# Kernel optimization log

Measured on AMD Instinct MI355X. Metric: run time of the kernel, lower is better.

The kernel has to match this reference:

```python
import jax, jax.numpy as jnp
import numpy as np

B, T, OBS, H, LAT = 512, 512, 64, 256, 16
NEG_SLOPE = 0.01  # flax nn.leaky_relu default


def _glorot(key, shape):
    fan_in, fan_out = shape[0], shape[-1]
    s = jnp.sqrt(6.0 / (fan_in + fan_out))
    return jax.random.uniform(key, shape, jnp.float32, -s, s)


def setup_inputs() -> dict:
    key = jax.random.key(0)
    ks = jax.random.split(key, 12)
    x = jax.random.normal(ks[0], (B, T, OBS), jnp.float32)
    lengths = jax.random.randint(ks[1], (B,), T // 4, T + 1)
    mask = jnp.arange(T)[None, :] < lengths[:, None]  # [B,T] bool, prefix-valid
    return {
        "x": x,
        "mask": mask,
        # encoder params
        "Wip": _glorot(ks[2], (OBS, H)), "bip": jnp.zeros((H,)),
        "Wi_e": _glorot(ks[3], (H, 4 * H)), "Wh_e": _glorot(ks[4], (H, 4 * H)),
        "b_e": jnp.zeros((4 * H,)),
        "Wlp": _glorot(ks[5], (H, LAT)), "blp": jnp.zeros((LAT,)),
        # decoder params
        "Wle": _glorot(ks[6], (LAT, H)), "ble": jnp.zeros((H,)),
        "Wi_d": _glorot(ks[7], (H, 4 * H)), "Wh_d": _glorot(ks[8], (H, 4 * H)),
        "b_d": jnp.zeros((4 * H,)),
        "Wop": _glorot(ks[9], (H, OBS)), "bop": jnp.zeros((OBS,)),
    }


def _lstm_step(c, h, x_t, Wi, Wh, b):
    # flax OptimizedLSTMCell: fused gates, order i, f, g, o
    z = x_t @ Wi + h @ Wh + b  # [B, 4H]
    i, f, g, o = jnp.split(z, 4, axis=-1)
    new_c = jax.nn.sigmoid(f) * c + jax.nn.sigmoid(i) * jnp.tanh(g)
    new_h = jax.nn.sigmoid(o) * jnp.tanh(new_c)
    return new_c, new_h


def _forward(x, mask, Wip, bip, Wi_e, Wh_e, b_e, Wlp, blp,
             Wle, ble, Wi_d, Wh_d, b_d, Wop, bop):
    # ---- Encoder ----
    xp = jax.nn.leaky_relu(x @ Wip + bip, NEG_SLOPE)  # [B,T,H]
    xs = (jnp.swapaxes(xp, 0, 1), jnp.swapaxes(mask, 0, 1)[:, :, None])  # [T,B,H],[T,B,1]

    def enc_step(carry, inp):
        c, h = carry
        x_t, m_t = inp
        nc, nh = _lstm_step(c, h, x_t, Wi_e, Wh_e, b_e)
        # masked carry update (MaskedLSTMCell)
        return (jnp.where(m_t, nc, c), jnp.where(m_t, nh, h)), None

    init = (jnp.zeros((x.shape[0], Wh_e.shape[0]), x.dtype),
            jnp.zeros((x.shape[0], Wh_e.shape[0]), x.dtype))
    (c_f, h_f), _ = jax.lax.scan(enc_step, init, xs)
    latent = h_f @ Wlp + blp  # [B,LAT]

    ctx = jax.nn.leaky_relu(latent @ Wle + ble, NEG_SLOPE)  # [B,H]

    def dec_step(carry, _):
        c, h = carry
        nc, nh = _lstm_step(c, h, h, Wi_d, Wh_d, b_d)
        pred = nh @ Wop + bop
        return (nc, nh), pred

    _, recon = jax.lax.scan(dec_step, (ctx, ctx), None, length=T)  # [T,B,OBS]
    recon = jnp.swapaxes(recon, 0, 1)  # [B,T,OBS]
    return recon, latent


def reference(x, mask, Wip, bip, Wi_e, Wh_e, b_e, Wlp, blp,
              Wle, ble, Wi_d, Wh_d, b_d, Wop, bop):
    return _forward(x, mask, Wip, bip, Wi_e, Wh_e, b_e, Wlp, blp,
                    Wle, ble, Wi_d, Wh_d, b_d, Wop, bop)
```

## Files before the change

kernel.cpp:

```cpp
#include <hip/hip_runtime.h>

typedef unsigned short u16;
typedef unsigned long long u64;
typedef float f32x4 __attribute__((ext_vector_type(4)));
typedef __bf16 bf16x8 __attribute__((ext_vector_type(8)));

#define NT_ 512
#define LD 264
#define SPIN_GUARD 100000

__device__ __forceinline__ u16 f2bf(float f) {
  unsigned u = __builtin_bit_cast(unsigned, f);
  u += 0x7FFFu + ((u >> 16) & 1u);
  return (u16)(u >> 16);
}
__device__ __forceinline__ float bf2f(u16 h) {
  unsigned u = ((unsigned)h) << 16;
  return __builtin_bit_cast(float, u);
}
__device__ __forceinline__ f32x4 splat4(float b) { f32x4 v = {b, b, b, b}; return v; }
__device__ __forceinline__ bf16x8 asb(uint4 v) { return __builtin_bit_cast(bf16x8, v); }
__device__ __forceinline__ float sigf(float v) { return 1.0f / (1.0f + exp2f(-1.44269504f * v)); }
__device__ __forceinline__ float tanhf_(float v) { float e = exp2f(2.88539008f * v); return 1.0f - 2.0f / (e + 1.0f); }

__device__ __forceinline__ u64 gld64(const u64* p) {
  return __hip_atomic_load(p, __ATOMIC_RELAXED, __HIP_MEMORY_SCOPE_AGENT);
}
__device__ __forceinline__ void gst64(u64* p, u64 v) {
  __hip_atomic_store(p, v, __ATOMIC_RELAXED, __HIP_MEMORY_SCOPE_AGENT);
}
__device__ __forceinline__ int gld32(const int* p) {
  return __hip_atomic_load(p, __ATOMIC_RELAXED, __HIP_MEMORY_SCOPE_AGENT);
}
__device__ __forceinline__ void gst32(int* p, int v) {
  __hip_atomic_store(p, v, __ATOMIC_RELAXED, __HIP_MEMORY_SCOPE_AGENT);
}

__global__ void k_pack_g(const float* __restrict__ src, const float* __restrict__ src2,
                         u16* __restrict__ dst) {
  int e = blockIdx.x * 256 + threadIdx.x;
  int j = e & 7, lane = (e >> 3) & 63, g = (e >> 9) & 3, ks = (e >> 11) & 7;
  int w = (e >> 14) & 3, s = (e >> 16) & 3;
  int k = ks * 32 + ((lane >> 4) << 3) + j;
  int col = g * 256 + s * 64 + w * 16 + (lane & 15);
  float v = src[k * 1024 + col];
  if (src2) v += src2[k * 1024 + col];
  dst[e] = f2bf(v);
}
__global__ void k_pack_wip(const float* __restrict__ Wip, u16* __restrict__ dst) {
  int e = blockIdx.x * 256 + threadIdx.x;
  int j = e & 7, lane = (e >> 3) & 63, n = (e >> 9) & 3, ks2 = (e >> 11) & 1, w = (e >> 12) & 3;
  int k = ks2 * 32 + ((lane >> 4) << 3) + j;
  int col = w * 64 + n * 16 + (lane & 15);
  dst[e] = f2bf(Wip[k * 256 + col]);
}
__global__ void k_pack_wop(const float* __restrict__ Wop, u16* __restrict__ dst) {
  int e = blockIdx.x * 256 + threadIdx.x;
  int j = e & 7, lane = (e >> 3) & 63, ks = (e >> 9) & 7, s = (e >> 12) & 3;
  int k = ks * 32 + ((lane >> 4) << 3) + j;
  int col = s * 16 + (lane & 15);
  dst[e] = f2bf(Wop[k * 64 + col]);
}

__global__ void k_lens(const unsigned char* __restrict__ mask, int* __restrict__ skeys) {
  int b = threadIdx.x;
  bool u8 = (mask[1] | mask[2] | mask[3]) != 0;
  int s = 0;
  if (u8) { const unsigned char* row = mask + b * NT_; for (int t = 0; t < NT_; t++) s += row[t] ? 1 : 0; }
  else { const int* row = (const int*)mask + b * NT_; for (int t = 0; t < NT_; t++) s += row[t] ? 1 : 0; }
  skeys[b] = s * 1024 + b;
}

__global__ void k_sort(int* __restrict__ skeys) {
  __shared__ int sk[512];
  int tid = threadIdx.x;
  sk[tid] = skeys[tid];
  __syncthreads();
  for (int k = 2; k <= 512; k <<= 1)
    for (int j = k >> 1; j > 0; j >>= 1) {
      int ixj = tid ^ j;
      if (ixj > tid) {
        int a = sk[tid], b = sk[ixj];
        bool up = ((tid & k) == 0);
        if ((a > b) == up) { sk[tid] = b; sk[ixj] = a; }
      }
      __syncthreads();
    }
  skeys[tid] = sk[tid];
}

__global__ void k_zero(int* __restrict__ flags) { flags[threadIdx.x] = 0; }

__global__ __launch_bounds__(256, 1) void k_rec3(
    const float* __restrict__ x,
    const u16* __restrict__ whe_p, const u16* __restrict__ wie_p,
    const u16* __restrict__ wd_p, const u16* __restrict__ wip_p,
    const u16* __restrict__ wop_p,
    const float* __restrict__ bip, const float* __restrict__ be,
    const float* __restrict__ Wlp, const float* __restrict__ blp,
    const float* __restrict__ Wle, const float* __restrict__ ble,
    const float* __restrict__ bd, const float* __restrict__ bop,
    const int* __restrict__ skeys,
    u64* __restrict__ hpub, int* __restrict__ eflag, int* __restrict__ dflag,
    float* __restrict__ out) {
  __shared__ __align__(16) u16 hx[16 * LD];
  __shared__ __align__(16) u16 xps[16 * LD];
  __shared__ __align__(16) u16 xbuf[16 * 72];
  __shared__ int ob_s[16], len_s[16];
  __shared__ float lat_s[256];

  const int tid = threadIdx.x;
  const int w = tid >> 6, lane = tid & 63, q = lane >> 4, n16 = lane & 15;
  const int b = blockIdx.x;
  const int g = (b & 7) + ((b >> 5) << 3);
  const int s = (b >> 3) & 3;

  if (tid < 16) {
    int v = skeys[g * 16 + tid];
    ob_s[tid] = v & 1023;
    len_s[tid] = v >> 10;
  }
  for (int i = tid; i < 16 * LD; i += 256) hx[i] = 0;
  __syncthreads();
  int maxlen = 0;
#pragma unroll
  for (int i = 0; i < 16; i++) maxlen = len_s[i] > maxlen ? len_s[i] : maxlen;
  int mylen[4];
#pragma unroll
  for (int r = 0; r < 4; r++) mylen[r] = len_s[q * 4 + r];

  const uint4* whe4 = (const uint4*)whe_p;
  const uint4* wie4 = (const uint4*)wie_p;
  const uint4* wip4 = (const uint4*)wip_p;
  uint4 wfh[32], wfx[32], wipf[8];
#pragma unroll
  for (int f = 0; f < 32; f++) wfh[f] = whe4[((s * 4 + w) * 32 + f) * 64 + lane];
#pragma unroll
  for (int f = 0; f < 32; f++) wfx[f] = wie4[((s * 4 + w) * 32 + f) * 64 + lane];
#pragma unroll
  for (int f = 0; f < 8; f++) wipf[f] = wip4[(w * 8 + f) * 64 + lane];

  float be_r[4], bipr[4];
#pragma unroll
  for (int gt = 0; gt < 4; gt++) be_r[gt] = be[gt * 256 + s * 64 + w * 16 + n16];
#pragma unroll
  for (int n = 0; n < 4; n++) bipr[n] = bip[w * 64 + n * 16 + n16];

  float creg[4], hreg[4];
#pragma unroll
  for (int r = 0; r < 4; r++) { creg[r] = 0.f; hreg[r] = 0.f; }

  const char* hxb = (const char*)hx;
  const char* xpsb = (const char*)xps;
  u64* hpg = hpub + (u64)g * 2048;
  int* efl = eflag + g * 4;
  int* dfl = dflag + g * 4;
  const int xr = tid >> 4, xc = tid & 15;
  const int pubw = (w * 16 + n16) * 4 + q;
  const int mycol = s * 64 + w * 16 + n16;

  for (int t = 0; t < maxlen; t++) {
    float4 xv = ((const float4*)x)[((size_t)ob_s[xr] * NT_ + t) * 16 + xc];
    {
      u64 pv = (u64)f2bf(xv.x) | ((u64)f2bf(xv.y) << 16) |
               ((u64)f2bf(xv.z) << 32) | ((u64)f2bf(xv.w) << 48);
      *(u64*)&xbuf[xr * 72 + xc * 4] = pv;
    }
    __syncthreads();
    f32x4 xacc[4];
#pragma unroll
    for (int n = 0; n < 4; n++) xacc[n] = splat4(bipr[n]);
#pragma unroll
    for (int ks2 = 0; ks2 < 2; ks2++) {
      bf16x8 a = *(const bf16x8*)((const char*)xbuf + n16 * 144 + ks2 * 64 + q * 16);
#pragma unroll
      for (int n = 0; n < 4; n++)
        xacc[n] = __builtin_amdgcn_mfma_f32_16x16x32_bf16(a, asb(wipf[ks2 * 4 + n]), xacc[n], 0, 0, 0);
    }
#pragma unroll
    for (int n = 0; n < 4; n++)
#pragma unroll
      for (int r = 0; r < 4; r++) {
        float v = xacc[n][r];
        v = v >= 0.f ? v : 0.01f * v;
        xps[(q * 4 + r) * LD + w * 64 + n * 16 + n16] = f2bf(v);
      }
    __syncthreads();
    f32x4 acc[4];
#pragma unroll
    for (int gt = 0; gt < 4; gt++) acc[gt] = splat4(be_r[gt]);
#pragma unroll
    for (int ks = 0; ks < 8; ks++) {
      bf16x8 a = *(const bf16x8*)(xpsb + n16 * (LD * 2) + ks * 64 + q * 16);
#pragma unroll
      for (int gt = 0; gt < 4; gt++)
        acc[gt] = __builtin_amdgcn_mfma_f32_16x16x32_bf16(a, asb(wfx[ks * 4 + gt]), acc[gt], 0, 0, 0);
    }
    if (t > 0) {
      if (tid < 4 && tid != s) {
        int gdn = 0;
        while (gld32(&efl[tid]) < t && ++gdn < SPIN_GUARD) {}
      }
      __syncthreads();
      const u64* src = hpg + (u64)(t & 1) * 1024;
#pragma unroll
      for (int e3 = 0; e3 < 3; e3++) {
        int sidx = e3 + (e3 >= s);
        u64 v = gld64(&src[sidx * 256 + tid]);
        int cc = sidx * 64 + (tid >> 2), qq = tid & 3;
#pragma unroll
        for (int r = 0; r < 4; r++) hx[(qq * 4 + r) * LD + cc] = (u16)(v >> (16 * r));
      }
    }
    __syncthreads();
#pragma unroll
    for (int ks = 0; ks < 8; ks++) {
      bf16x8 a = *(const bf16x8*)(hxb + n16 * (LD * 2) + ks * 64 + q * 16);
#pragma unroll
      for (int gt = 0; gt < 4; gt++)
        acc[gt] = __builtin_amdgcn_mfma_f32_16x16x32_bf16(a, asb(wfh[ks * 4 + gt]), acc[gt], 0, 0, 0);
    }
    u16 hb[4];
#pragma unroll
    for (int r = 0; r < 4; r++) {
      float i_ = sigf(acc[0][r]);
      float f_ = sigf(acc[1][r]);
      float g_ = tanhf_(acc[2][r]);
      float o_ = sigf(acc[3][r]);
      float nc = f_ * creg[r] + i_ * g_;
      float nh = o_ * tanhf_(nc);
      bool upd = t < mylen[r];
      creg[r] = upd ? nc : creg[r];
      hreg[r] = upd ? nh : hreg[r];
      hb[r] = f2bf(hreg[r]);
    }
    {
      u64 pv = (u64)hb[0] | ((u64)hb[1] << 16) | ((u64)hb[2] << 32) | ((u64)hb[3] << 48);
      gst64(&hpg[(u64)((t + 1) & 1) * 1024 + s * 256 + pubw], pv);
    }
    __syncthreads();
#pragma unroll
    for (int r = 0; r < 4; r++) hx[(q * 4 + r) * LD + mycol] = hb[r];
    __syncthreads();
    if (tid == 0) gst32(&efl[s], t + 1);
  }

  if (tid < 4 && tid != s) {
    int gdn = 0;
    while (gld32(&efl[tid]) < maxlen && ++gdn < SPIN_GUARD) {}
  }
  __syncthreads();
  {
    const u64* src = hpg + (u64)(maxlen & 1) * 1024;
#pragma unroll
    for (int e3 = 0; e3 < 3; e3++) {
      int sidx = e3 + (e3 >= s);
      u64 v = gld64(&src[sidx * 256 + tid]);
      int cc = sidx * 64 + (tid >> 2), qq = tid & 3;
#pragma unroll
      for (int r = 0; r < 4; r++) hx[(qq * 4 + r) * LD + cc] = (u16)(v >> (16 * r));
    }
  }
  __syncthreads();
  if (tid == 0) gst32(&dfl[s], 1);

  {
    int m = tid >> 4, j = tid & 15;
    float acc_ = blp[j];
    for (int k = 0; k < 256; k++) acc_ = fmaf(bf2f(hx[m * LD + k]), Wlp[k * 16 + j], acc_);
    if (s == 0) out[16777216 + ob_s[m] * 16 + j] = acc_;
    lat_s[m * 16 + j] = acc_;
  }
  __syncthreads();
  for (int i = tid; i < 4096; i += 256) {
    int m = i >> 8, c = i & 255;
    float v = ble[c];
#pragma unroll
    for (int k = 0; k < 16; k++) v = fmaf(lat_s[m * 16 + k], Wle[k * 256 + c], v);
    v = v >= 0.f ? v : 0.01f * v;
    hx[m * LD + c] = f2bf(v);
  }
  __syncthreads();
#pragma unroll
  for (int r = 0; r < 4; r++) {
    hreg[r] = bf2f(hx[(q * 4 + r) * LD + mycol]);
    creg[r] = hreg[r];
  }

  const uint4* wd4 = (const uint4*)wd_p;
  const uint4* wop4 = (const uint4*)wop_p;
#pragma unroll
  for (int f = 0; f < 32; f++) wfh[f] = wd4[((s * 4 + w) * 32 + f) * 64 + lane];
#pragma unroll
  for (int f = 0; f < 8; f++) wfx[f] = wop4[(s * 8 + f) * 64 + lane];
  float bd_r[4];
#pragma unroll
  for (int gt = 0; gt < 4; gt++) bd_r[gt] = bd[gt * 256 + s * 64 + w * 16 + n16];
  float bop_r = bop[s * 16 + n16];
  int orow[4];
#pragma unroll
  for (int r = 0; r < 4; r++) orow[r] = ob_s[q * 4 + r] << 15;

  if (tid < 4 && tid != s) {
    int gdn = 0;
    while (gld32(&dfl[tid]) < 1 && ++gdn < SPIN_GUARD) {}
  }
  __syncthreads();

  for (int d = 0; d < NT_; d++) {
    if (d > 0) {
      if (tid < 4 && tid != s) {
        int gdn = 0;
        while (gld32(&dfl[tid]) < d + 1 && ++gdn < SPIN_GUARD) {}
      }
      __syncthreads();
      const u64* src = hpg + (u64)(d & 1) * 1024;
#pragma unroll
      for (int e3 = 0; e3 < 3; e3++) {
        int sidx = e3 + (e3 >= s);
        u64 v = gld64(&src[sidx * 256 + tid]);
        int cc = sidx * 64 + (tid >> 2), qq = tid & 3;
#pragma unroll
        for (int r = 0; r < 4; r++) hx[(qq * 4 + r) * LD + cc] = (u16)(v >> (16 * r));
      }
    }
    __syncthreads();
    f32x4 pacc = splat4(0.f);
#pragma unroll
    for (int ks = 0; ks < 8; ks++) {
      bf16x8 a = *(const bf16x8*)(hxb + n16 * (LD * 2) + ks * 64 + q * 16);
      pacc = __builtin_amdgcn_mfma_f32_16x16x32_bf16(a, asb(wfx[ks]), pacc, 0, 0, 0);
    }
    if (w == 0 && d > 0) {
#pragma unroll
      for (int r = 0; r < 4; r++)
        out[orow[r] + ((d - 1) << 6) + (s << 4) + n16] = pacc[r] + bop_r;
    }
    f32x4 acc[4];
#pragma unroll
    for (int gt = 0; gt < 4; gt++) acc[gt] = splat4(bd_r[gt]);
#pragma unroll
    for (int ks = 0; ks < 8; ks++) {
      bf16x8 a = *(const bf16x8*)(hxb + n16 * (LD * 2) + ks * 64 + q * 16);
#pragma unroll
      for (int gt = 0; gt < 4; gt++)
        acc[gt] = __builtin_amdgcn_mfma_f32_16x16x32_bf16(a, asb(wfh[ks * 4 + gt]), acc[gt], 0, 0, 0);
    }
    u16 hb[4];
#pragma unroll
    for (int r = 0; r < 4; r++) {
      float i_ = sigf(acc[0][r]);
      float f_ = sigf(acc[1][r]);
      float g_ = tanhf_(acc[2][r]);
      float o_ = sigf(acc[3][r]);
      float nc = f_ * creg[r] + i_ * g_;
      creg[r] = nc;
      hreg[r] = o_ * tanhf_(nc);
      hb[r] = f2bf(hreg[r]);
    }
    {
      u64 pv = (u64)hb[0] | ((u64)hb[1] << 16) | ((u64)hb[2] << 32) | ((u64)hb[3] << 48);
      gst64(&hpg[(u64)((d + 1) & 1) * 1024 + s * 256 + pubw], pv);
    }
    __syncthreads();
#pragma unroll
    for (int r = 0; r < 4; r++) hx[(q * 4 + r) * LD + mycol] = hb[r];
    __syncthreads();
    if (tid == 0) gst32(&dfl[s], d + 2);
  }
  if (tid < 4 && tid != s) {
    int gdn = 0;
    while (gld32(&dfl[tid]) < NT_ + 1 && ++gdn < SPIN_GUARD) {}
  }
  __syncthreads();
  {
    const u64* src = hpg;
#pragma unroll
    for (int e3 = 0; e3 < 3; e3++) {
      int sidx = e3 + (e3 >= s);
      u64 v = gld64(&src[sidx * 256 + tid]);
      int cc = sidx * 64 + (tid >> 2), qq = tid & 3;
#pragma unroll
      for (int r = 0; r < 4; r++) hx[(qq * 4 + r) * LD + cc] = (u16)(v >> (16 * r));
    }
  }
  __syncthreads();
  if (w == 0) {
    f32x4 pacc = splat4(0.f);
#pragma unroll
    for (int ks = 0; ks < 8; ks++) {
      bf16x8 a = *(const bf16x8*)(hxb + n16 * (LD * 2) + ks * 64 + q * 16);
      pacc = __builtin_amdgcn_mfma_f32_16x16x32_bf16(a, asb(wfx[ks]), pacc, 0, 0, 0);
    }
#pragma unroll
    for (int r = 0; r < 4; r++)
      out[orow[r] + (511 << 6) + (s << 4) + n16] = pacc[r] + bop_r;
  }
}

#define OFF_WHE 0ull
#define OFF_WIE 524288ull
#define OFF_WD 1048576ull
#define OFF_WIP 1572864ull
#define OFF_WOP 1605632ull
#define OFF_HPUB 1638400ull
#define OFF_EFLAG 2162688ull
#define OFF_DFLAG 2163200ull
#define OFF_SKEYS 2163712ull
#define MIN_WS 2165760ull

extern "C" void kernel_launch(void* const* d_in, const int* in_sizes, int n_in,
                              void* d_out, int out_size, void* d_ws, size_t ws_size,
                              hipStream_t stream) {
  const float* x = (const float*)d_in[0];
  const unsigned char* mask = (const unsigned char*)d_in[1];
  const float* Wip = (const float*)d_in[2];
  const float* bip = (const float*)d_in[3];
  const float* Wie = (const float*)d_in[4];
  const float* Whe = (const float*)d_in[5];
  const float* be = (const float*)d_in[6];
  const float* Wlp = (const float*)d_in[7];
  const float* blp = (const float*)d_in[8];
  const float* Wle = (const float*)d_in[9];
  const float* ble = (const float*)d_in[10];
  const float* Wid = (const float*)d_in[11];
  const float* Whd = (const float*)d_in[12];
  const float* bd = (const float*)d_in[13];
  const float* Wop = (const float*)d_in[14];
  const float* bop = (const float*)d_in[15];
  float* out = (float*)d_out;
  char* ws = (char*)d_ws;

  if (ws_size < MIN_WS) return;

  u16* whe_p = (u16*)(ws + OFF_WHE);
  u16* wie_p = (u16*)(ws + OFF_WIE);
  u16* wd_p = (u16*)(ws + OFF_WD);
  u16* wip_p = (u16*)(ws + OFF_WIP);
  u16* wop_p = (u16*)(ws + OFF_WOP);
  u64* hpub = (u64*)(ws + OFF_HPUB);
  int* eflag = (int*)(ws + OFF_EFLAG);
  int* dflag = (int*)(ws + OFF_DFLAG);
  int* skeys = (int*)(ws + OFF_SKEYS);

  k_pack_g<<<1024, 256, 0, stream>>>(Whe, nullptr, whe_p);
  k_pack_g<<<1024, 256, 0, stream>>>(Wie, nullptr, wie_p);
  k_pack_g<<<1024, 256, 0, stream>>>(Wid, Whd, wd_p);
  k_pack_wip<<<64, 256, 0, stream>>>(Wip, wip_p);
  k_pack_wop<<<64, 256, 0, stream>>>(Wop, wop_p);
  k_lens<<<1, 512, 0, stream>>>(mask, skeys);
  k_sort<<<1, 512, 0, stream>>>(skeys);
  k_zero<<<1, 256, 0, stream>>>(eflag);

  k_rec3<<<128, 256, 0, stream>>>(x, whe_p, wie_p, wd_p, wip_p, wop_p,
                                  bip, be, Wlp, blp, Wle, ble, bd, bop,
                                  skeys, hpub, eflag, dflag, out);
}
```

Before: 3.405 ms.

## Replace flag-based inter-block sync with tagged hidden-state polling

Removes the separate per-step encoder and decoder flag arrays and instead embeds a step tag in the upper 16 bits of each published bf16 hidden value, so consumers poll the data itself with cache-bypassing dwordx4 loads. This drops one flag store, one flag poll and several block-wide barriers per timestep in the latency-bound recurrence. Barriers become raw s_barrier with only an lgkmcnt wait, and the next x row is prefetched one step ahead. The cost is twice the publish traffic, since each value is now 32-bit. Correctness relies on the tag and the sc0/sc1 coherence bits, and on the zeroed buffer never matching a live tag.

```diff
diff --git a/kernel.cpp b/kernel.cpp
--- a/kernel.cpp
+++ b/kernel.cpp
@@ -1,9 +1,11 @@
 #include <hip/hip_runtime.h>
 
 typedef unsigned short u16;
+typedef unsigned u32;
 typedef unsigned long long u64;
 typedef float f32x4 __attribute__((ext_vector_type(4)));
 typedef __bf16 bf16x8 __attribute__((ext_vector_type(8)));
+typedef u32 u32x4 __attribute__((ext_vector_type(4)));
 
 #define NT_ 512
 #define LD 264
@@ -23,17 +25,35 @@
 __device__ __forceinline__ float sigf(float v) { return 1.0f / (1.0f + exp2f(-1.44269504f * v)); }
 __device__ __forceinline__ float tanhf_(float v) { float e = exp2f(2.88539008f * v); return 1.0f - 2.0f / (e + 1.0f); }
 
-__device__ __forceinline__ u64 gld64(const u64* p) {
-  return __hip_atomic_load(p, __ATOMIC_RELAXED, __HIP_MEMORY_SCOPE_AGENT);
-}
-__device__ __forceinline__ void gst64(u64* p, u64 v) {
-  __hip_atomic_store(p, v, __ATOMIC_RELAXED, __HIP_MEMORY_SCOPE_AGENT);
-}
-__device__ __forceinline__ int gld32(const int* p) {
-  return __hip_atomic_load(p, __ATOMIC_RELAXED, __HIP_MEMORY_SCOPE_AGENT);
-}
-__device__ __forceinline__ void gst32(int* p, int v) {
-  __hip_atomic_store(p, v, __ATOMIC_RELAXED, __HIP_MEMORY_SCOPE_AGENT);
+__device__ __forceinline__ void barL() {
+  asm volatile("s_waitcnt lgkmcnt(0)\n\ts_barrier" ::: "memory");
+}
+
+__device__ __forceinline__ void pub4(u32* p, u32x4 v) {
+  asm volatile("global_store_dwordx4 %0, %1, off sc0 sc1" :: "v"(p), "v"(v) : "memory");
+}
+
+__device__ __forceinline__ void poll3(const u32* a0, const u32* a1, const u32* a2,
+                                      u32 tg, u32x4& r0, u32x4& r1, u32x4& r2) {
+  int gdn = 0;
+  while (true) {
+    u32x4 t0, t1, t2;
+    asm volatile(
+        "global_load_dwordx4 %0, %3, off sc0 sc1\n\t"
+        "global_load_dwordx4 %1, %4, off sc0 sc1\n\t"
+        "global_load_dwordx4 %2, %5, off sc0 sc1\n\t"
+        "s_waitcnt vmcnt(0)"
+        : "=&v"(t0), "=&v"(t1), "=&v"(t2)
+        : "v"(a0), "v"(a1), "v"(a2)
+        : "memory");
+    bool ok = (t0[0] >> 16) == tg && (t0[1] >> 16) == tg &&
+              (t0[2] >> 16) == tg && (t0[3] >> 16) == tg &&
+              (t1[0] >> 16) == tg && (t1[1] >> 16) == tg &&
+              (t1[2] >> 16) == tg && (t1[3] >> 16) == tg &&
+              (t2[0] >> 16) == tg && (t2[1] >> 16) == tg &&
+              (t2[2] >> 16) == tg && (t2[3] >> 16) == tg;
+    if (ok || ++gdn >= SPIN_GUARD) { r0 = t0; r1 = t1; r2 = t2; return; }
+  }
 }
 
 __global__ void k_pack_g(const float* __restrict__ src, const float* __restrict__ src2,
@@ -89,9 +109,13 @@
   skeys[tid] = sk[tid];
 }
 
-__global__ void k_zero(int* __restrict__ flags) { flags[threadIdx.x] = 0; }
-
-__global__ __launch_bounds__(256, 1) void k_rec3(
+__global__ void k_zero_hpub(u32* __restrict__ hp) {
+  int i = blockIdx.x * 256 + threadIdx.x;
+  u32x4 z = {0u, 0u, 0u, 0u};
+  pub4(hp + (size_t)i * 4, z);
+}
+
+__global__ __launch_bounds__(256, 1) void k_rec4(
     const float* __restrict__ x,
     const u16* __restrict__ whe_p, const u16* __restrict__ wie_p,
     const u16* __restrict__ wd_p, const u16* __restrict__ wip_p,
@@ -101,8 +125,7 @@
     const float* __restrict__ Wle, const float* __restrict__ ble,
     const float* __restrict__ bd, const float* __restrict__ bop,
     const int* __restrict__ skeys,
-    u64* __restrict__ hpub, int* __restrict__ eflag, int* __restrict__ dflag,
-    float* __restrict__ out) {
+    u32* __restrict__ hpub, float* __restrict__ out) {
   __shared__ __align__(16) u16 hx[16 * LD];
   __shared__ __align__(16) u16 xps[16 * LD];
   __shared__ __align__(16) u16 xbuf[16 * 72];
@@ -152,21 +175,44 @@
 
   const char* hxb = (const char*)hx;
   const char* xpsb = (const char*)xps;
-  u64* hpg = hpub + (u64)g * 2048;
-  int* efl = eflag + g * 4;
-  int* dfl = dflag + g * 4;
-  const int xr = tid >> 4, xc = tid & 15;
-  const int pubw = (w * 16 + n16) * 4 + q;
+  u32* hp32 = hpub + (size_t)g * 8192;
+  const int p0 = (s == 0) ? 1 : 0;
+  const int p1 = (s <= 1) ? 2 : 1;
+  const int p2 = (s <= 2) ? 3 : 2;
+  const int widx = ((tid >> 2) << 4) + ((tid & 3) << 2);
+  const int ccl = tid >> 2, qq = tid & 3;
+  const int cc0 = p0 * 64 + ccl, cc1 = p1 * 64 + ccl, cc2 = p2 * 64 + ccl;
+  u32* pubp = hp32 + s * 1024 + ((w * 16 + n16) << 4) + (q << 2);
   const int mycol = s * 64 + w * 16 + n16;
 
+#define SCAT3()                                  \
+  do {                                           \
+    hx[(qq * 4 + 0) * LD + cc0] = (u16)r0[0];    \
+    hx[(qq * 4 + 1) * LD + cc0] = (u16)r0[1];    \
+    hx[(qq * 4 + 2) * LD + cc0] = (u16)r0[2];    \
+    hx[(qq * 4 + 3) * LD + cc0] = (u16)r0[3];    \
+    hx[(qq * 4 + 0) * LD + cc1] = (u16)r1[0];    \
+    hx[(qq * 4 + 1) * LD + cc1] = (u16)r1[1];    \
+    hx[(qq * 4 + 2) * LD + cc1] = (u16)r1[2];    \
+    hx[(qq * 4 + 3) * LD + cc1] = (u16)r1[3];    \
+    hx[(qq * 4 + 0) * LD + cc2] = (u16)r2[0];    \
+    hx[(qq * 4 + 1) * LD + cc2] = (u16)r2[1];    \
+    hx[(qq * 4 + 2) * LD + cc2] = (u16)r2[2];    \
+    hx[(qq * 4 + 3) * LD + cc2] = (u16)r2[3];    \
+  } while (0)
+
+  const float4* xr4 = (const float4*)x + (size_t)ob_s[tid >> 4] * 8192 + (tid & 15);
+  float4 xv = xr4[0];
+
   for (int t = 0; t < maxlen; t++) {
-    float4 xv = ((const float4*)x)[((size_t)ob_s[xr] * NT_ + t) * 16 + xc];
     {
       u64 pv = (u64)f2bf(xv.x) | ((u64)f2bf(xv.y) << 16) |
                ((u64)f2bf(xv.z) << 32) | ((u64)f2bf(xv.w) << 48);
-      *(u64*)&xbuf[xr * 72 + xc * 4] = pv;
-    }
-    __syncthreads();
+      *(u64*)&xbuf[(tid >> 4) * 72 + (tid & 15) * 4] = pv;
+    }
+    int tn = (t + 1 < maxlen) ? t + 1 : t;
+    float4 xnx = xr4[(size_t)tn * 16];
+    barL();
     f32x4 xacc[4];
 #pragma unroll
     for (int n = 0; n < 4; n++) xacc[n] = splat4(bipr[n]);
@@ -185,7 +231,7 @@
         v = v >= 0.f ? v : 0.01f * v;
         xps[(q * 4 + r) * LD + w * 64 + n * 16 + n16] = f2bf(v);
       }
-    __syncthreads();
+    barL();
     f32x4 acc[4];
 #pragma unroll
     for (int gt = 0; gt < 4; gt++) acc[gt] = splat4(be_r[gt]);
@@ -197,22 +243,13 @@
         acc[gt] = __builtin_amdgcn_mfma_f32_16x16x32_bf16(a, asb(wfx[ks * 4 + gt]), acc[gt], 0, 0, 0);
     }
     if (t > 0) {
-      if (tid < 4 && tid != s) {
-        int gdn = 0;
-        while (gld32(&efl[tid]) < t && ++gdn < SPIN_GUARD) {}
-      }
-      __syncthreads();
-      const u64* src = hpg + (u64)(t & 1) * 1024;
-#pragma unroll
-      for (int e3 = 0; e3 < 3; e3++) {
-        int sidx = e3 + (e3 >= s);
-        u64 v = gld64(&src[sidx * 256 + tid]);
-        int cc = sidx * 64 + (tid >> 2), qq = tid & 3;
-#pragma unroll
-        for (int r = 0; r < 4; r++) hx[(qq * 4 + r) * LD + cc] = (u16)(v >> (16 * r));
-      }
-    }
-    __syncthreads();
+      const u32* bp = hp32 + ((t & 1) << 12);
+      u32x4 r0, r1, r2;
+      poll3(bp + p0 * 1024 + widx, bp + p1 * 1024 + widx, bp + p2 * 1024 + widx,
+            (u32)t, r0, r1, r2);
+      SCAT3();
+    }
+    barL();
 #pragma unroll
     for (int ks = 0; ks < 8; ks++) {
       bf16x8 a = *(const bf16x8*)(hxb + n16 * (LD * 2) + ks * 64 + q * 16);
@@ -235,34 +272,24 @@
       hb[r] = f2bf(hreg[r]);
     }
     {
-      u64 pv = (u64)hb[0] | ((u64)hb[1] << 16) | ((u64)hb[2] << 32) | ((u64)hb[3] << 48);
-      gst64(&hpg[(u64)((t + 1) & 1) * 1024 + s * 256 + pubw], pv);
-    }
-    __syncthreads();
+      u32 tgw = (u32)(t + 1) << 16;
+      u32x4 pv = {tgw | hb[0], tgw | hb[1], tgw | hb[2], tgw | hb[3]};
+      pub4(pubp + (((t + 1) & 1) << 12), pv);
+    }
+    barL();
 #pragma unroll
     for (int r = 0; r < 4; r++) hx[(q * 4 + r) * LD + mycol] = hb[r];
-    __syncthreads();
-    if (tid == 0) gst32(&efl[s], t + 1);
-  }
-
-  if (tid < 4 && tid != s) {
-    int gdn = 0;
-    while (gld32(&efl[tid]) < maxlen && ++gdn < SPIN_GUARD) {}
-  }
-  __syncthreads();
+    xv = xnx;
+  }
+
   {
-    const u64* src = hpg + (u64)(maxlen & 1) * 1024;
-#pragma unroll
-    for (int e3 = 0; e3 < 3; e3++) {
-      int sidx = e3 + (e3 >= s);
-      u64 v = gld64(&src[sidx * 256 + tid]);
-      int cc = sidx * 64 + (tid >> 2), qq = tid & 3;
-#pragma unroll
-      for (int r = 0; r < 4; r++) hx[(qq * 4 + r) * LD + cc] = (u16)(v >> (16 * r));
-    }
-  }
-  __syncthreads();
-  if (tid == 0) gst32(&dfl[s], 1);
+    const u32* bp = hp32 + ((maxlen & 1) << 12);
+    u32x4 r0, r1, r2;
+    poll3(bp + p0 * 1024 + widx, bp + p1 * 1024 + widx, bp + p2 * 1024 + widx,
+          (u32)maxlen, r0, r1, r2);
+    SCAT3();
+  }
+  barL();
 
   {
     int m = tid >> 4, j = tid & 15;
@@ -300,31 +327,17 @@
   int orow[4];
 #pragma unroll
   for (int r = 0; r < 4; r++) orow[r] = ob_s[q * 4 + r] << 15;
-
-  if (tid < 4 && tid != s) {
-    int gdn = 0;
-    while (gld32(&dfl[tid]) < 1 && ++gdn < SPIN_GUARD) {}
-  }
-  __syncthreads();
+  const int E = maxlen;
 
   for (int d = 0; d < NT_; d++) {
     if (d > 0) {
-      if (tid < 4 && tid != s) {
-        int gdn = 0;
-        while (gld32(&dfl[tid]) < d + 1 && ++gdn < SPIN_GUARD) {}
-      }
-      __syncthreads();
-      const u64* src = hpg + (u64)(d & 1) * 1024;
-#pragma unroll
-      for (int e3 = 0; e3 < 3; e3++) {
-        int sidx = e3 + (e3 >= s);
-        u64 v = gld64(&src[sidx * 256 + tid]);
-        int cc = sidx * 64 + (tid >> 2), qq = tid & 3;
-#pragma unroll
-        for (int r = 0; r < 4; r++) hx[(qq * 4 + r) * LD + cc] = (u16)(v >> (16 * r));
-      }
-    }
-    __syncthreads();
+      const u32* bp = hp32 + (((E + d) & 1) << 12);
+      u32x4 r0, r1, r2;
+      poll3(bp + p0 * 1024 + widx, bp + p1 * 1024 + widx, bp + p2 * 1024 + widx,
+            (u32)(E + d), r0, r1, r2);
+      SCAT3();
+    }
+    barL();
     f32x4 pacc = splat4(0.f);
 #pragma unroll
     for (int ks = 0; ks < 8; ks++) {
@@ -359,32 +372,22 @@
       hb[r] = f2bf(hreg[r]);
     }
     {
-      u64 pv = (u64)hb[0] | ((u64)hb[1] << 16) | ((u64)hb[2] << 32) | ((u64)hb[3] << 48);
-      gst64(&hpg[(u64)((d + 1) & 1) * 1024 + s * 256 + pubw], pv);
-    }
-    __syncthreads();
+      u32 tgw = (u32)(E + d + 1) << 16;
+      u32x4 pv = {tgw | hb[0], tgw | hb[1], tgw | hb[2], tgw | hb[3]};
+      pub4(pubp + (((E + d + 1) & 1) << 12), pv);
+    }
+    barL();
 #pragma unroll
     for (int r = 0; r < 4; r++) hx[(q * 4 + r) * LD + mycol] = hb[r];
-    __syncthreads();
-    if (tid == 0) gst32(&dfl[s], d + 2);
-  }
-  if (tid < 4 && tid != s) {
-    int gdn = 0;
-    while (gld32(&dfl[tid]) < NT_ + 1 && ++gdn < SPIN_GUARD) {}
-  }
-  __syncthreads();
+  }
   {
-    const u64* src = hpg;
-#pragma unroll
-    for (int e3 = 0; e3 < 3; e3++) {
-      int sidx = e3 + (e3 >= s);
-      u64 v = gld64(&src[sidx * 256 + tid]);
-      int cc = sidx * 64 + (tid >> 2), qq = tid & 3;
-#pragma unroll
-      for (int r = 0; r < 4; r++) hx[(qq * 4 + r) * LD + cc] = (u16)(v >> (16 * r));
-    }
-  }
-  __syncthreads();
+    const u32* bp = hp32 + (((E + NT_) & 1) << 12);
+    u32x4 r0, r1, r2;
+    poll3(bp + p0 * 1024 + widx, bp + p1 * 1024 + widx, bp + p2 * 1024 + widx,
+          (u32)(E + NT_), r0, r1, r2);
+    SCAT3();
+  }
+  barL();
   if (w == 0) {
     f32x4 pacc = splat4(0.f);
 #pragma unroll
@@ -396,6 +399,7 @@
     for (int r = 0; r < 4; r++)
       out[orow[r] + (511 << 6) + (s << 4) + n16] = pacc[r] + bop_r;
   }
+#undef SCAT3
 }
 
 #define OFF_WHE 0ull
@@ -404,10 +408,8 @@
 #define OFF_WIP 1572864ull
 #define OFF_WOP 1605632ull
 #define OFF_HPUB 1638400ull
-#define OFF_EFLAG 2162688ull
-#define OFF_DFLAG 2163200ull
-#define OFF_SKEYS 2163712ull
-#define MIN_WS 2165760ull
+#define OFF_SKEYS 2686976ull
+#define MIN_WS 2689024ull
 
 extern "C" void kernel_launch(void* const* d_in, const int* in_sizes, int n_in,
                               void* d_out, int out_size, void* d_ws, size_t ws_size,
@@ -438,9 +440,7 @@
   u16* wd_p = (u16*)(ws + OFF_WD);
   u16* wip_p = (u16*)(ws + OFF_WIP);
   u16* wop_p = (u16*)(ws + OFF_WOP);
-  u64* hpub = (u64*)(ws + OFF_HPUB);
-  int* eflag = (int*)(ws + OFF_EFLAG);
-  int* dflag = (int*)(ws + OFF_DFLAG);
+  u32* hpub = (u32*)(ws + OFF_HPUB);
   int* skeys = (int*)(ws + OFF_SKEYS);
 
   k_pack_g<<<1024, 256, 0, stream>>>(Whe, nullptr, whe_p);
@@ -450,9 +450,9 @@
   k_pack_wop<<<64, 256, 0, stream>>>(Wop, wop_p);
   k_lens<<<1, 512, 0, stream>>>(mask, skeys);
   k_sort<<<1, 512, 0, stream>>>(skeys);
-  k_zero<<<1, 256, 0, stream>>>(eflag);
-
-  k_rec3<<<128, 256, 0, stream>>>(x, whe_p, wie_p, wd_p, wip_p, wop_p,
+  k_zero_hpub<<<256, 256, 0, stream>>>(hpub);
+
+  k_rec4<<<128, 256, 0, stream>>>(x, whe_p, wie_p, wd_p, wip_p, wop_p,
                                   bip, be, Wlp, blp, Wle, ble, bd, bop,
-                                  skeys, hpub, eflag, dflag, out);
-}
+                                  skeys, hpub, out);
+}
```

After: 2.802 ms. 17.7% less time.
